# Performance work log

Measured on AMD Instinct MI355X. Metric: run time of the kernel, lower is better.

The kernel has to match this reference:

```python
import jax, jax.numpy as jnp
import numpy as np

B, L, D = 4, 2048, 1024
H, DK, DV, CS = 4, 128, 256, 16  # heads, head_qk_dim, head_v_dim, chunk_size
KD, VD = H * DK, H * DV          # 512, 1024
CONV = 4
EPS = 1e-5


def silu(x):
    return x * jax.nn.sigmoid(x)


def setup_inputs():
    key = jax.random.key(0)
    ks = jax.random.split(key, 9)
    s = 0.02
    return {
        "hidden_states": jax.random.normal(ks[0], (B, L, D), jnp.float32),
        "conv_w": jax.random.normal(ks[1], (D, CONV), jnp.float32) * 0.2,
        "Wq": jax.random.normal(ks[2], (KD, D), jnp.float32) * s,
        "Wk": jax.random.normal(ks[3], (KD, D), jnp.float32) * s,
        "Wv": jax.random.normal(ks[4], (VD, D), jnp.float32) * s,
        "Wb": jax.random.normal(ks[5], (H, D), jnp.float32) * s,
        "Wg": jax.random.normal(ks[6], (VD, D), jnp.float32) * s,
        "Wo": jax.random.normal(ks[7], (D, VD), jnp.float32) * s,
        "norm_w": jnp.ones((DV,), jnp.float32),
    }


def short_conv(x, w):
    # causal depthwise conv1d with SiLU activation: x [B,L,D], w [D,K]
    K = w.shape[1]
    xp = jnp.pad(x, ((0, 0), (K - 1, 0), (0, 0)))
    y = sum(xp[:, j:j + x.shape[1], :] * w[:, j] for j in range(K))
    return silu(y)


def delta_rule_chunk(q, k, v, beta):
    # fused_chunk_delta_rule: q,k [B,H,L,DK], v [B,H,L,DV], beta [B,H,L]
    b, h, l, dk = q.shape
    dv = v.shape[-1]
    nc = l // CS
    k = k * jax.lax.rsqrt(jnp.sum(k * k, -1, keepdims=True) + 1e-12)  # L2-normalize keys
    q = q * (dk ** -0.5)
    qc = q.reshape(b, h, nc, CS, dk)
    kc = k.reshape(b, h, nc, CS, dk)
    vc = v.reshape(b, h, nc, CS, dv)
    bc = beta.reshape(b, h, nc, CS)
    kb = kc * bc[..., None]
    # WY representation: T = (I + strict_tril(diag(beta) K K^T))^{-1}
    A = jnp.einsum('bhncd,bhnmd->bhncm', kb, kc)
    strict = jnp.tril(jnp.ones((CS, CS), q.dtype), -1)
    M = jnp.eye(CS, dtype=q.dtype) + A * strict
    eye = jnp.broadcast_to(jnp.eye(CS, dtype=q.dtype), M.shape)
    T = jax.scipy.linalg.solve_triangular(M, eye, lower=True)
    w = jnp.einsum('bhncm,bhnmd->bhncd', T, kb)
    u = jnp.einsum('bhncm,bhnmd->bhncd', T, vc * bc[..., None])
    causal = jnp.tril(jnp.ones((CS, CS), q.dtype))

    def step(S, inp):
        qi, ki, wi, ui = inp  # [B,H,CS,dk/dv]
        u_adj = ui - jnp.einsum('bhcd,bhdv->bhcv', wi, S)
        attn = jnp.einsum('bhcd,bhmd->bhcm', qi, ki) * causal
        o = jnp.einsum('bhcd,bhdv->bhcv', qi, S) + jnp.einsum('bhcm,bhmv->bhcv', attn, u_adj)
        S = S + jnp.einsum('bhcd,bhcv->bhdv', ki, u_adj)
        return S, o

    xs = tuple(jnp.moveaxis(t, 2, 0) for t in (qc, kc, w, u))
    S0 = jnp.zeros((b, h, dk, dv), q.dtype)
    _, os_ = jax.lax.scan(step, S0, xs)
    return jnp.moveaxis(os_, 0, 2).reshape(b, h, l, dv)


def reference(hidden_states, conv_w, Wq, Wk, Wv, Wb, Wg, Wo, norm_w):
    x = short_conv(hidden_states, conv_w)
    q = (x @ Wq.T).reshape(B, L, H, DK).transpose(0, 2, 1, 3)
    k = (x @ Wk.T).reshape(B, L, H, DK).transpose(0, 2, 1, 3)
    v = (x @ Wv.T).reshape(B, L, H, DV).transpose(0, 2, 1, 3)
    beta = jax.nn.sigmoid(x @ Wb.T).transpose(0, 2, 1)  # [B,H,L]
    o = delta_rule_chunk(q, k, v, beta)                 # [B,H,L,DV]
    o = o.transpose(0, 2, 1, 3)                          # [B,L,H,DV]
    g = (x @ Wg.T).reshape(B, L, H, DV)
    o = o * jax.lax.rsqrt(jnp.mean(o * o, -1, keepdims=True) + EPS) * norm_w * silu(g)
    return o.reshape(B, L, VD) @ Wo.T
```

## Files before the change

kernel.cpp:

```cpp
#include <hip/hip_runtime.h>
#include <cstdint>
#include <cstddef>

typedef _Float16 f16;
typedef _Float16 f16x4 __attribute__((ext_vector_type(4)));
typedef _Float16 f16x8 __attribute__((ext_vector_type(8)));
typedef float floatx4 __attribute__((ext_vector_type(4)));

#define MFMA32(a,b,c) __builtin_amdgcn_mfma_f32_16x16x32_f16((a),(b),(c),0,0,0)

#define ROWS 8192
#define NCHUNK 128
static constexpr float QSCALE = 0.08838834764831845f;

static __device__ __forceinline__ float sigmoidf_(float x) { return 1.0f / (1.0f + expf(-x)); }

static __device__ __forceinline__ uint32_t pack2(f16 a, f16 b) {
  union { f16 h[2]; uint32_t u; } v; v.h[0] = a; v.h[1] = b; return v.u;
}

#define GLOAD_LDS(gptr, lptr)                                                  \
  __builtin_amdgcn_global_load_lds(                                            \
      (const __attribute__((address_space(1))) void*)(gptr),                   \
      (__attribute__((address_space(3))) void*)(lptr), 16, 0, 0)

#define WAITV(N) do { asm volatile("s_waitcnt vmcnt(" #N ")" ::: "memory");    \
                      __builtin_amdgcn_sched_barrier(0); } while (0)

#define SBAR() __builtin_amdgcn_sched_barrier(0)

__global__ __launch_bounds__(256) void wconv_kernel(
    const float* __restrict__ Wq, const float* __restrict__ Wk,
    const float* __restrict__ Wv, const float* __restrict__ Wg,
    const float* __restrict__ Wo,
    f16* __restrict__ WcatHi, f16* __restrict__ WcatLoKV, f16* __restrict__ WoHi) {
  int tid = blockIdx.x * 256 + threadIdx.x;
  int e8 = tid * 8;
  if (e8 < 3145728) {
    int row = e8 >> 10, col = e8 & 1023;
    const float* src;
    if (row < 512)       src = Wk + (size_t)row * 1024 + col;
    else if (row < 1536) src = Wv + (size_t)(row - 512) * 1024 + col;
    else if (row < 2048) src = Wq + (size_t)(row - 1536) * 1024 + col;
    else                 src = Wg + (size_t)(row - 2048) * 1024 + col;
    f16 thi[8] __attribute__((aligned(16)));
    f16 tlo[8] __attribute__((aligned(16)));
#pragma unroll
    for (int j = 0; j < 8; j++) {
      float x = src[j];
      f16 h = (f16)x;
      thi[j] = h;
      tlo[j] = (f16)(x - (float)h);
    }
    *(uint4*)&WcatHi[e8] = *(const uint4*)thi;
    if (row < 1536) *(uint4*)&WcatLoKV[e8] = *(const uint4*)tlo;
  } else {
    int idx = e8 - 3145728;
    f16 t[8] __attribute__((aligned(16)));
#pragma unroll
    for (int j = 0; j < 8; j++) t[j] = (f16)Wo[idx + j];
    *(uint4*)&WoHi[idx] = *(const uint4*)t;
  }
}

__global__ __launch_bounds__(256) void conv_kernel(
    const float* __restrict__ hs, const float* __restrict__ cw,
    f16* __restrict__ xhi, f16* __restrict__ xlo) {
  int row = blockIdx.x;
  int b = row >> 11, l = row & 2047;
  int d = threadIdx.x * 4;
  floatx4 w0 = *(const floatx4*)&cw[(d + 0) * 4];
  floatx4 w1 = *(const floatx4*)&cw[(d + 1) * 4];
  floatx4 w2 = *(const floatx4*)&cw[(d + 2) * 4];
  floatx4 w3 = *(const floatx4*)&cw[(d + 3) * 4];
  floatx4 acc = {0.f, 0.f, 0.f, 0.f};
#pragma unroll
  for (int j = 0; j < 4; j++) {
    int ls = l - 3 + j;
    if (ls < 0) continue;
    floatx4 hv = *(const floatx4*)&hs[(size_t)(b * 2048 + ls) * 1024 + d];
    acc[0] += hv[0] * w0[j];
    acc[1] += hv[1] * w1[j];
    acc[2] += hv[2] * w2[j];
    acc[3] += hv[3] * w3[j];
  }
  f16 ohi[4] __attribute__((aligned(8)));
  f16 olo[4] __attribute__((aligned(8)));
#pragma unroll
  for (int q = 0; q < 4; q++) {
    float y = acc[q] * sigmoidf_(acc[q]);
    f16 h = (f16)y;
    ohi[q] = h;
    olo[q] = (f16)(y - (float)h);
  }
  *(uint2*)&xhi[(size_t)row * 1024 + d] = *(const uint2*)ohi;
  *(uint2*)&xlo[(size_t)row * 1024 + d] = *(const uint2*)olo;
}

__global__ __launch_bounds__(256) void beta_kernel(
    const f16* __restrict__ xhi, const f16* __restrict__ xlo,
    const float* __restrict__ Wb, float* __restrict__ betaf) {
  int row = blockIdx.x;
  int t = threadIdx.x;
  __shared__ floatx4 red[256];
  int c = t * 4;
  float xv[4];
#pragma unroll
  for (int j = 0; j < 4; j++)
    xv[j] = (float)xhi[(size_t)row * 1024 + c + j] + (float)xlo[(size_t)row * 1024 + c + j];
  floatx4 p = {0.f, 0.f, 0.f, 0.f};
#pragma unroll
  for (int hh = 0; hh < 4; hh++) {
    const float* wr = Wb + hh * 1024 + c;
    p[hh] = xv[0] * wr[0] + xv[1] * wr[1] + xv[2] * wr[2] + xv[3] * wr[3];
  }
  red[t] = p;
  __syncthreads();
  for (int s = 128; s > 0; s >>= 1) {
    if (t < s) red[t] += red[t + s];
    __syncthreads();
  }
  if (t < 4) betaf[(size_t)row * 4 + t] = sigmoidf_(red[0][t]);
}

__global__ __launch_bounds__(256) void gemm_hilo_kv(
    const f16* __restrict__ Ahi, const f16* __restrict__ Alo,
    const f16* __restrict__ Bhi, const f16* __restrict__ Blo,
    f16* __restrict__ ChHi, f16* __restrict__ ChLo, int K) {
  __shared__ __attribute__((aligned(16))) f16 AsH[4096];
  __shared__ __attribute__((aligned(16))) f16 AsL[4096];
  __shared__ __attribute__((aligned(16))) f16 BsH[4096];
  __shared__ __attribute__((aligned(16))) f16 BsL[4096];
  const int t = threadIdx.x;
  const int lane = t & 63, wave = t >> 6;
  const int lc = lane & 15, quad = lane >> 4;
  const int wm = (wave >> 1) * 64, wn = (wave & 1) * 64;
  const int m0 = blockIdx.y * 128, n0 = blockIdx.x * 128;
  const int scol = ((lane & 3) ^ ((lane >> 3) & 3)) * 8;
  int srow[2];
#pragma unroll
  for (int pp = 0; pp < 2; pp++) srow[pp] = (wave * 2 + pp) * 16 + (lane >> 2);
  const int swz = (quad ^ ((lc >> 1) & 3)) * 8;
  floatx4 acc[4][4] = {};
  for (int kt = 0; kt < K; kt += 32) {
    __syncthreads();
#pragma unroll
    for (int pp = 0; pp < 2; pp++) {
      int ldso = (wave * 2 + pp) * 512;
      GLOAD_LDS(&Ahi[(size_t)(m0 + srow[pp]) * K + kt + scol], AsH + ldso);
      GLOAD_LDS(&Alo[(size_t)(m0 + srow[pp]) * K + kt + scol], AsL + ldso);
      GLOAD_LDS(&Bhi[(size_t)(n0 + srow[pp]) * K + kt + scol], BsH + ldso);
      GLOAD_LDS(&Blo[(size_t)(n0 + srow[pp]) * K + kt + scol], BsL + ldso);
    }
    __syncthreads();
    f16x8 ah[4], al[4], bh2[4], bl[4];
#pragma unroll
    for (int i = 0; i < 4; i++) {
      ah[i] = *(const f16x8*)&AsH[(wm + i * 16 + lc) * 32 + swz];
      al[i] = *(const f16x8*)&AsL[(wm + i * 16 + lc) * 32 + swz];
    }
#pragma unroll
    for (int j = 0; j < 4; j++) {
      bh2[j] = *(const f16x8*)&BsH[(wn + j * 16 + lc) * 32 + swz];
      bl[j]  = *(const f16x8*)&BsL[(wn + j * 16 + lc) * 32 + swz];
    }
#pragma unroll
    for (int i = 0; i < 4; i++)
#pragma unroll
      for (int j = 0; j < 4; j++) {
        acc[i][j] = MFMA32(ah[i], bh2[j], acc[i][j]);
        acc[i][j] = MFMA32(al[i], bh2[j], acc[i][j]);
        acc[i][j] = MFMA32(ah[i], bl[j], acc[i][j]);
      }
  }
#pragma unroll
  for (int i = 0; i < 4; i++)
#pragma unroll
    for (int j = 0; j < 4; j++)
#pragma unroll
      for (int rr = 0; rr < 4; rr++) {
        int row = m0 + wm + i * 16 + quad * 4 + rr;
        int col = n0 + wn + j * 16 + lc;
        float x = acc[i][j][rr];
        f16 h = (f16)x;
        ChHi[(size_t)row * 3072 + col] = h;
        ChLo[(size_t)row * 1536 + col] = (f16)(x - (float)h);
      }
}

template <int OUTF16>
__global__ __launch_bounds__(256) void gemm_plain(
    const f16* __restrict__ A, const f16* __restrict__ Bw,
    f16* __restrict__ Ch, float* __restrict__ Cf, int K, int ldc) {
  __shared__ __attribute__((aligned(16))) f16 As[4096];
  __shared__ __attribute__((aligned(16))) f16 Bs[4096];
  const int t = threadIdx.x;
  const int lane = t & 63, wave = t >> 6;
  const int lc = lane & 15, quad = lane >> 4;
  const int wm = (wave >> 1) * 64, wn = (wave & 1) * 64;
  const int m0 = blockIdx.y * 128, n0 = blockIdx.x * 128;
  const int scol = ((lane & 3) ^ ((lane >> 3) & 3)) * 8;
  int srow[2];
#pragma unroll
  for (int pp = 0; pp < 2; pp++) srow[pp] = (wave * 2 + pp) * 16 + (lane >> 2);
  const int swz = (quad ^ ((lc >> 1) & 3)) * 8;
  floatx4 acc[4][4] = {};
  for (int kt = 0; kt < K; kt += 32) {
    __syncthreads();
#pragma unroll
    for (int pp = 0; pp < 2; pp++) {
      int ldso = (wave * 2 + pp) * 512;
      GLOAD_LDS(&A[(size_t)(m0 + srow[pp]) * K + kt + scol],  As + ldso);
      GLOAD_LDS(&Bw[(size_t)(n0 + srow[pp]) * K + kt + scol], Bs + ldso);
    }
    __syncthreads();
    f16x8 af[4], bf[4];
#pragma unroll
    for (int i = 0; i < 4; i++) af[i] = *(const f16x8*)&As[(wm + i * 16 + lc) * 32 + swz];
#pragma unroll
    for (int j = 0; j < 4; j++) bf[j] = *(const f16x8*)&Bs[(wn + j * 16 + lc) * 32 + swz];
#pragma unroll
    for (int i = 0; i < 4; i++)
#pragma unroll
      for (int j = 0; j < 4; j++) acc[i][j] = MFMA32(af[i], bf[j], acc[i][j]);
  }
#pragma unroll
  for (int i = 0; i < 4; i++)
#pragma unroll
    for (int j = 0; j < 4; j++)
#pragma unroll
      for (int rr = 0; rr < 4; rr++) {
        int row = m0 + wm + i * 16 + quad * 4 + rr;
        int col = n0 + wn + j * 16 + lc;
        if (OUTF16) Ch[(size_t)row * ldc + col] = (f16)acc[i][j][rr];
        else        Cf[(size_t)row * ldc + col] = acc[i][j][rr];
      }
}

__global__ __launch_bounds__(256) void prepass_kernel(
    const f16* __restrict__ qkvgHi, const f16* __restrict__ kvLo,
    const float* __restrict__ betaf,
    f16* __restrict__ wHi, f16* __restrict__ wLo,
    f16* __restrict__ kTHi, f16* __restrict__ kTLo,
    f16* __restrict__ uHi, f16* __restrict__ uLo,
    float* __restrict__ attno) {
  int bid = blockIdx.x;
  int bh = bid >> 7, n = bid & 127;
  int b = bh >> 2, h = bh & 3;
  int t = threadIdx.x;

  __shared__ __attribute__((aligned(16))) float kc[16][132];
  __shared__ __attribute__((aligned(16))) float qc[16][132];
  __shared__ __attribute__((aligned(16))) float vb[16][260];
  __shared__ float Mm[16][16];
  __shared__ float Tt[16][16];
  __shared__ float Tb[16][16];
  __shared__ float part[16][16];
  __shared__ float betas[16];
  __shared__ float nrm[16];

  const size_t rowbase = (size_t)(b * 2048 + n * 16);
  {
    int i = t >> 4, o8 = (t & 15) * 8;
    size_t oh = (rowbase + i) * 3072;
    size_t ol = (rowbase + i) * 1536;
#pragma unroll
    for (int j = 0; j < 8; j++)
      kc[i][o8 + j] = (float)qkvgHi[oh + h * 128 + o8 + j] +
                      (float)kvLo[ol + h * 128 + o8 + j];
#pragma unroll
    for (int j = 0; j < 8; j++)
      qc[i][o8 + j] = (float)qkvgHi[oh + 1536 + h * 128 + o8 + j];
  }
  if (t < 16) betas[t] = betaf[(rowbase + t) * 4 + h];
  __syncthreads();
  {
    int i = t >> 4, sg = t & 15;
    float s = 0.f;
#pragma unroll
    for (int j = 0; j < 8; j++) { float v = kc[i][sg * 8 + j]; s += v * v; }
    part[i][sg] = s;
  }
  __syncthreads();
  if (t < 16) {
    float s = 0.f;
#pragma unroll
    for (int j = 0; j < 16; j++) s += part[t][j];
    nrm[t] = rsqrtf(s + 1e-12f);
  }
  __syncthreads();
  {
    int i = t >> 4, o8 = (t & 15) * 8;
    float sc = nrm[i];
#pragma unroll
    for (int j = 0; j < 8; j++) kc[i][o8 + j] *= sc;
  }
  __syncthreads();
  {
    int d = t & 127, ih = t >> 7;
    f16 thi[8] __attribute__((aligned(16)));
    f16 tlo[8] __attribute__((aligned(16)));
#pragma unroll
    for (int j = 0; j < 8; j++) {
      float x = kc[ih * 8 + j][d];
      f16 hh = (f16)x;
      thi[j] = hh;
      tlo[j] = (f16)(x - (float)hh);
    }
    size_t base = ((size_t)bh * 128 + n) * 2048 + d * 16 + ih * 8;
    *(uint4*)&kTHi[base] = *(const uint4*)thi;
    *(uint4*)&kTLo[base] = *(const uint4*)tlo;
  }
  {
    int i = t >> 4, j = t & 15;
    float s = 0.f;
    for (int x = 0; x < 128; x += 4)
      s += kc[i][x] * kc[j][x] + kc[i][x + 1] * kc[j][x + 1] +
           kc[i][x + 2] * kc[j][x + 2] + kc[i][x + 3] * kc[j][x + 3];
    Mm[i][j] = (i == j ? 1.f : 0.f) + ((j < i) ? betas[i] * s : 0.f);
  }
  __syncthreads();
  if (t < 16) {
    int j = t;
    float Tc[16];
#pragma unroll
    for (int i = 0; i < 16; i++) Tc[i] = 0.f;
    Tc[j] = 1.f;
    for (int i = j + 1; i < 16; i++) {
      float s = 0.f;
      for (int k2 = j; k2 < i; k2++) s += Mm[i][k2] * Tc[k2];
      Tc[i] = -s;
    }
    for (int i = 0; i < 16; i++) Tt[i][j] = Tc[i];
  }
  __syncthreads();
  { int i = t >> 4, m = t & 15; Tb[i][m] = Tt[i][m] * betas[m]; }
  {
    int m = t >> 4, c16 = (t & 15) * 16;
    size_t oh = (rowbase + m) * 3072 + 512 + h * 256 + c16;
    size_t ol = (rowbase + m) * 1536 + 512 + h * 256 + c16;
    float bm = betas[m];
#pragma unroll
    for (int j = 0; j < 16; j++)
      vb[m][c16 + j] = bm * ((float)qkvgHi[oh + j] + (float)kvLo[ol + j]);
  }
  __syncthreads();
  {
    int i = t >> 4, dg = t & 15;
    f16 thi[8] __attribute__((aligned(16)));
    f16 tlo[8] __attribute__((aligned(16)));
#pragma unroll
    for (int dd = 0; dd < 8; dd++) {
      int d = dg * 8 + dd;
      float s = 0.f;
#pragma unroll
      for (int m = 0; m < 16; m++) s += Tb[i][m] * kc[m][d];
      s = -s;
      f16 hh = (f16)s;
      thi[dd] = hh;
      tlo[dd] = (f16)(s - (float)hh);
    }
    size_t base = ((size_t)bh * 128 + n) * 2048 + i * 128 + dg * 8;
    *(uint4*)&wHi[base] = *(const uint4*)thi;
    *(uint4*)&wLo[base] = *(const uint4*)tlo;
  }
  {
    int v = t;
    f16 thi[16] __attribute__((aligned(16)));
    f16 tlo[16] __attribute__((aligned(16)));
#pragma unroll
    for (int i = 0; i < 16; i++) {
      float s2 = 0.f;
#pragma unroll
      for (int m = 0; m < 16; m++) s2 += Tt[i][m] * vb[m][v];
      f16 hh = (f16)s2;
      thi[i] = hh;
      tlo[i] = (f16)(s2 - (float)hh);
    }
    size_t base = ((((size_t)(v >> 4) * 16 + bh) * 128 + n) * 16 + (v & 15)) * 16;
    ((uint4*)&uHi[base])[0] = ((const uint4*)thi)[0];
    ((uint4*)&uHi[base])[1] = ((const uint4*)thi)[1];
    ((uint4*)&uLo[base])[0] = ((const uint4*)tlo)[0];
    ((uint4*)&uLo[base])[1] = ((const uint4*)tlo)[1];
  }
  {
    int i = t >> 4, j = t & 15;
    float s = 0.f;
    for (int x = 0; x < 128; x++) s += qc[i][x] * kc[j][x];
    attno[((size_t)bh * 128 + n) * 256 + i * 16 + j] = (j <= i) ? QSCALE * s : 0.f;
  }
}

#define STG_W   0
#define STG_WL  2048
#define STG_Q   4096
#define STG_KH  6144
#define STG_KL  8192
#define STG_SZ  10240

__global__ __launch_bounds__(64, 1) void scan_kernel(
    const f16* __restrict__ qkvgHi,
    const f16* __restrict__ wHi, const f16* __restrict__ wLo,
    const f16* __restrict__ kTHi, const f16* __restrict__ kTLo,
    const float* __restrict__ attn,
    const f16* __restrict__ uHi, const f16* __restrict__ uLo,
    float* __restrict__ o1, float* __restrict__ o2) {
  const int bid = blockIdx.x;
  const int slc = bid >> 4, bh = bid & 15;
  const int b = bh >> 2, h = bh & 3;
  const int v0 = slc * 16;
  const int lane = threadIdx.x;
  const int lc = lane & 15, quad = lane >> 4;
  const int qh = quad & 1;

  __shared__ __attribute__((aligned(16))) f16 stg[2][STG_SZ];
  __shared__ __attribute__((aligned(16))) f16 S_hi[16][136];
  __shared__ __attribute__((aligned(16))) f16 S_lo[16][136];

  floatx4 accS[8] = {};

  const size_t cb = (size_t)bh * 128;
  const f16* qb = qkvgHi + (size_t)b * 2048 * 3072 + 1536 + h * 128;
  const f16* ubH = uHi + ((size_t)(slc * 16 + bh)) * 128 * 256 + lc * 16 + quad * 4;
  const f16* ubL = uLo + ((size_t)(slc * 16 + bh)) * 128 * 256 + lc * 16 + quad * 4;
  const float* ab = attn + cb * 256 + lc * 16 + qh * 8;
  float* ob = (bh < 12) ? (o1 + (size_t)bh * 2048 * 256)
                        : (o2 + (size_t)(bh - 12) * 2048 * 256);

  int woff[4], koff[4], qoff[4];
#pragma unroll
  for (int p = 0; p < 4; p++) {
    int cid = p * 64 + lane;
    int row = cid >> 4, dgs = (cid & 15) ^ (row & 7);
    int d = cid >> 1,  ih = (cid & 1) ^ ((cid >> 3) & 1);
    woff[p] = row * 128 + dgs * 8;
    koff[p] = d * 16 + ih * 8;
    qoff[p] = row * 3072 + dgs * 8;
  }

  uint4 pa0[2], pa1[2];
  uint2 puh[2], pul[2];

  auto ISSUE_REG = [&](int slot, int nn) {
    pa0[slot] = *(const uint4*)(ab + (size_t)nn * 256);
    pa1[slot] = *(const uint4*)(ab + (size_t)nn * 256 + 4);
    puh[slot] = *(const uint2*)(ubH + (size_t)nn * 256);
    pul[slot] = *(const uint2*)(ubL + (size_t)nn * 256);
  };
  auto ISSUE_WQ = [&](int buf, int nn) {
    const f16* wsrc  = wHi + (cb + (size_t)nn) * 2048;
    const f16* wlsrc = wLo + (cb + (size_t)nn) * 2048;
    const f16* qsrc  = qb + (size_t)nn * 16 * 3072;
    f16* sbp = &stg[buf][0];
#pragma unroll
    for (int p = 0; p < 4; p++) {
      GLOAD_LDS(wsrc + woff[p],  sbp + STG_W  + p * 512);
      GLOAD_LDS(wlsrc + woff[p], sbp + STG_WL + p * 512);
      GLOAD_LDS(qsrc + qoff[p],  sbp + STG_Q  + p * 512);
    }
  };
  auto ISSUE_K = [&](int buf, int nn) {
    const f16* khsrc = kTHi + (cb + (size_t)nn) * 2048;
    const f16* klsrc = kTLo + (cb + (size_t)nn) * 2048;
    f16* sbp = &stg[buf][0];
#pragma unroll
    for (int p = 0; p < 4; p++) {
      GLOAD_LDS(khsrc + koff[p], sbp + STG_KH + p * 512);
      GLOAD_LDS(klsrc + koff[p], sbp + STG_KL + p * 512);
    }
  };

  ISSUE_REG(0, 0); ISSUE_WQ(0, 0); ISSUE_K(0, 0);
  ISSUE_REG(1, 1); ISSUE_WQ(1, 1); ISSUE_K(1, 1);

  for (int n = 0; n < NCHUNK; n += 2) {
#pragma unroll
    for (int hf = 0; hf < 2; hf++) {
      const int nn = n + hf;
      f16* sb = &stg[hf][0];

#pragma unroll
      for (int dt = 0; dt < 8; dt++) {
        f16x4 h4, l4;
#pragma unroll
        for (int r = 0; r < 4; r++) {
          float x = accS[dt][r];
          f16 hh = (f16)x;
          h4[r] = hh;
          l4[r] = (f16)(x - (float)hh);
        }
        *(f16x4*)&S_hi[lc][dt * 16 + quad * 4] = h4;
        *(f16x4*)&S_lo[lc][dt * 16 + quad * 4] = l4;
      }

      if (nn == 0)       WAITV(24);
      else if (nn < 127) WAITV(28);
      else               WAITV(4);

      floatx4 acc_u;
      {
        union { uint2 u2; f16 hh[4]; } Uh, Ul;
        Uh.u2 = puh[hf]; Ul.u2 = pul[hf];
#pragma unroll
        for (int r = 0; r < 4; r++) acc_u[r] = (float)Uh.hh[r] + (float)Ul.hh[r];
      }
      f16x8 aah, aal;
      {
        union { uint4 u4[2]; float f[8]; } PA;
        PA.u4[0] = pa0[hf]; PA.u4[1] = pa1[hf];
#pragma unroll
        for (int j = 0; j < 8; j++) {
          float a = PA.f[j];
          f16 ahh = (f16)a;
          aah[j] = ahh;
          aal[j] = (f16)(a - (float)ahh);
        }
      }
      if (nn + 2 < NCHUNK) ISSUE_REG(hf, nn + 2);

      f16x8 shf[4], slf[4], wah[4], wal[4], qah[4];
#pragma unroll
      for (int ks = 0; ks < 4; ks++) {
        shf[ks] = *(const f16x8*)&S_hi[lc][ks * 32 + quad * 8];
        slf[ks] = *(const f16x8*)&S_lo[lc][ks * 32 + quad * 8];
        int gi = lc * 128 + (((ks * 4 + quad) ^ (lc & 7)) * 8);
        wah[ks] = *(const f16x8*)(sb + STG_W  + gi);
        wal[ks] = *(const f16x8*)(sb + STG_WL + gi);
        qah[ks] = *(const f16x8*)(sb + STG_Q  + gi);
      }
      SBAR();
      if (nn + 2 < NCHUNK) ISSUE_WQ(hf, nn + 2);

      floatx4 a1 = {0.f, 0.f, 0.f, 0.f}, a2 = {0.f, 0.f, 0.f, 0.f};
#pragma unroll
      for (int ks = 0; ks < 4; ks++) {
        acc_u = MFMA32(wah[ks], shf[ks], acc_u);
        a1    = MFMA32(wah[ks], slf[ks], a1);
        a2    = MFMA32(wal[ks], shf[ks], a2);
      }
      acc_u = acc_u + a1 + a2;
      floatx4 acc_o = {0.f, 0.f, 0.f, 0.f};
#pragma unroll
      for (int ks = 0; ks < 4; ks++) acc_o = MFMA32(qah[ks], shf[ks], acc_o);
#pragma unroll
      for (int ks = 0; ks < 4; ks++) acc_o = MFMA32(qah[ks], slf[ks], acc_o);

      f16x8 ubf;
      {
        f16 h0 = (f16)acc_u[0], h1 = (f16)acc_u[1];
        f16 h2 = (f16)acc_u[2], h3 = (f16)acc_u[3];
        uint32_t uh01 = pack2(h0, h1), uh23 = pack2(h2, h3);
        uint32_t ul01 = pack2((f16)(acc_u[0] - (float)h0), (f16)(acc_u[1] - (float)h1));
        uint32_t ul23 = pack2((f16)(acc_u[2] - (float)h2), (f16)(acc_u[3] - (float)h3));
        int srcA = (2 * qh) * 16 + lc;
        int srcB = srcA + 16;
        uint32_t Ah0 = __shfl((int)uh01, srcA, 64), Ah1 = __shfl((int)uh23, srcA, 64);
        uint32_t Bh0 = __shfl((int)uh01, srcB, 64), Bh1 = __shfl((int)uh23, srcB, 64);
        uint32_t Al0 = __shfl((int)ul01, srcA, 64), Al1 = __shfl((int)ul23, srcA, 64);
        uint32_t Bl0 = __shfl((int)ul01, srcB, 64), Bl1 = __shfl((int)ul23, srcB, 64);
        union { uint32_t u[4]; f16x8 v; } U;
        bool hi = (quad < 2);
        U.u[0] = hi ? Ah0 : Al0;
        U.u[1] = hi ? Ah1 : Al1;
        U.u[2] = hi ? Bh0 : Bl0;
        U.u[3] = hi ? Bh1 : Bl1;
        ubf = U.v;
      }
#pragma unroll
      for (int r = 0; r < 4; r++) acc_o[r] *= QSCALE;
      acc_o = MFMA32(aah, ubf, acc_o);
      acc_o = MFMA32(aal, ubf, acc_o);
#pragma unroll
      for (int r = 0; r < 4; r++)
        ob[(size_t)(nn * 16 + quad * 4 + r) * 256 + v0 + lc] = acc_o[r];

      const int kswz = (qh ^ ((lc >> 2) & 1)) * 8 + lc * 16;
#pragma unroll
      for (int dt = 0; dt < 8; dt++) {
        f16x8 kah = *(const f16x8*)(sb + STG_KH + dt * 256 + kswz);
        f16x8 kal = *(const f16x8*)(sb + STG_KL + dt * 256 + kswz);
        accS[dt] = MFMA32(kah, ubf, accS[dt]);
        accS[dt] = MFMA32(kal, ubf, accS[dt]);
      }
      SBAR();
      if (nn + 2 < NCHUNK) ISSUE_K(hf, nn + 2);
    }
  }
}

__global__ __launch_bounds__(256) void gate_kernel(
    const float* __restrict__ o1, const float* __restrict__ o2,
    const f16* __restrict__ qkvgHi, const float* __restrict__ norm_w,
    f16* __restrict__ onh) {
  int h = threadIdx.x >> 6, lane = threadIdx.x & 63;
  int r = blockIdx.x;
  int b = r >> 11, l = r & 2047;
  int bh = b * 4 + h;
  const float* orow = ((bh < 12) ? (o1 + (size_t)bh * 524288)
                                 : (o2 + (size_t)(bh - 12) * 524288)) + (size_t)l * 256;
  int v = lane * 4;
  floatx4 ov = *(const floatx4*)&orow[v];
  float ss = ov[0] * ov[0] + ov[1] * ov[1] + ov[2] * ov[2] + ov[3] * ov[3];
  for (int m = 32; m > 0; m >>= 1) ss += __shfl_xor(ss, m);
  float rms = rsqrtf(ss * (1.0f / 256.0f) + 1e-5f);
  size_t goff = (size_t)r * 3072 + 2048 + h * 256 + v;
  floatx4 nw = *(const floatx4*)&norm_w[v];
  f16 outv[4] __attribute__((aligned(8)));
#pragma unroll
  for (int q2 = 0; q2 < 4; q2++) {
    float g = (float)qkvgHi[goff + q2];
    outv[q2] = (f16)(ov[q2] * rms * nw[q2] * (g * sigmoidf_(g)));
  }
  *(uint2*)&onh[(size_t)r * 1024 + h * 256 + v] = *(const uint2*)outv;
}

extern "C" void kernel_launch(void* const* d_in, const int* in_sizes, int n_in,
                              void* d_out, int out_size, void* d_ws, size_t ws_size,
                              hipStream_t stream) {
  (void)in_sizes; (void)n_in; (void)out_size; (void)ws_size;
  const float* hs     = (const float*)d_in[0];
  const float* conv_w = (const float*)d_in[1];
  const float* Wq     = (const float*)d_in[2];
  const float* Wk     = (const float*)d_in[3];
  const float* Wv     = (const float*)d_in[4];
  const float* Wb     = (const float*)d_in[5];
  const float* Wg     = (const float*)d_in[6];
  const float* Wo     = (const float*)d_in[7];
  const float* norm_w = (const float*)d_in[8];
  float* out = (float*)d_out;

  char* ws = (char*)d_ws;
  f16*   x_hi    = (f16*)(ws + 0);
  f16*   x_lo    = (f16*)(ws + 16777216);
  f16*   uHi     = (f16*)(ws + 0);
  f16*   uLo     = (f16*)(ws + 16777216);
  f16*   WcatHi  = (f16*)(ws + 33554432);
  float* o2f     = (float*)(ws + 33554432);
  f16*   WcatLo  = (f16*)(ws + 39845888);
  f16*   WoHi    = (f16*)(ws + 42991616);
  float* betaf   = (float*)(ws + 45088768);
  f16*   qkvgHi  = (f16*)(ws + 45219840);
  f16*   kvLo    = (f16*)(ws + 95551488);
  float* o1f     = (float*)(ws + 95551488);
  f16*   wHi     = (f16*)(ws + 120717312);
  f16*   on_h    = (f16*)(ws + 120717312);
  f16*   wLo     = (f16*)(ws + 129105920);
  f16*   kTHi    = (f16*)(ws + 137494528);
  f16*   kTLo    = (f16*)(ws + 145883136);
  float* attnf   = (float*)(ws + 154271744);

  wconv_kernel<<<2048, 256, 0, stream>>>(Wq, Wk, Wv, Wg, Wo, WcatHi, WcatLo, WoHi);
  conv_kernel<<<ROWS, 256, 0, stream>>>(hs, conv_w, x_hi, x_lo);
  beta_kernel<<<ROWS, 256, 0, stream>>>(x_hi, x_lo, Wb, betaf);
  gemm_hilo_kv<<<dim3(12, 64), 256, 0, stream>>>(
      x_hi, x_lo, WcatHi, WcatLo, qkvgHi, kvLo, 1024);
  gemm_plain<1><<<dim3(12, 64), 256, 0, stream>>>(
      x_hi, WcatHi + (size_t)1536 * 1024, qkvgHi + 1536, nullptr, 1024, 3072);
  prepass_kernel<<<16 * NCHUNK, 256, 0, stream>>>(
      qkvgHi, kvLo, betaf, wHi, wLo, kTHi, kTLo, uHi, uLo, attnf);
  scan_kernel<<<256, 64, 0, stream>>>(
      qkvgHi, wHi, wLo, kTHi, kTLo, attnf, uHi, uLo, o1f, o2f);
  gate_kernel<<<ROWS, 256, 0, stream>>>(o1f, o2f, qkvgHi, norm_w, on_h);
  gemm_plain<0><<<dim3(8, 64), 256, 0, stream>>>(
      on_h, WoHi, nullptr, out, 1024, 1024);
}
```

Measured before the change: 567.7 us.

## Process chunk pairs per scan step using precomputed cross-chunk correction matrices

```diff
diff --git a/kernel.cpp b/kernel.cpp
--- a/kernel.cpp
+++ b/kernel.cpp
@@ -11,6 +11,7 @@
 
 #define ROWS 8192
 #define NCHUNK 128
+#define NSUPER 64
 static constexpr float QSCALE = 0.08838834764831845f;
 
 static __device__ __forceinline__ float sigmoidf_(float x) { return 1.0f / (1.0f + expf(-x)); }
@@ -391,12 +392,55 @@
   }
 }
 
+__global__ __launch_bounds__(256) void cabd_kernel(
+    f16* qkvg,
+    const f16* __restrict__ wHi, const f16* __restrict__ wLo,
+    const f16* __restrict__ kTHi, const f16* __restrict__ kTLo) {
+  int bid = blockIdx.x;
+  int bh = bid >> 6, sc = bid & 63;
+  int b = bh >> 2, h = bh & 3;
+  int t = threadIdx.x;
+  int cA = 2 * sc, cB = 2 * sc + 1;
+  const size_t cb = (size_t)bh * 128;
+
+  __shared__ float wf[16][128];
+  __shared__ float qf[16][128];
+  __shared__ float kf[128][17];
+
+  {
+    int i = t >> 4, d0 = (t & 15) * 8;
+    size_t wbase = (cb + cB) * 2048 + i * 128 + d0;
+    size_t qbase = ((size_t)b * 2048 + cB * 16 + i) * 3072 + 1536 + h * 128 + d0;
+#pragma unroll
+    for (int j = 0; j < 8; j++) {
+      wf[i][d0 + j] = (float)wHi[wbase + j] + (float)wLo[wbase + j];
+      qf[i][d0 + j] = (float)qkvg[qbase + j];
+    }
+    int d = t >> 1, tk0 = (t & 1) * 8;
+    size_t kb = (cb + cA) * 2048 + d * 16 + tk0;
+#pragma unroll
+    for (int j = 0; j < 8; j++)
+      kf[d][tk0 + j] = (float)kTHi[kb + j] + (float)kTLo[kb + j];
+  }
+  __syncthreads();
+  int i = t >> 4, j = t & 15;
+  float sc1 = 0.f, sd1 = 0.f;
+  for (int d = 0; d < 128; d++) {
+    float kv = kf[d][j];
+    sc1 += wf[i][d] * kv;
+    sd1 += qf[i][d] * kv;
+  }
+  f16 ch = (f16)sc1, dh = (f16)sd1;
+  size_t o = (size_t)(bh * 64 + sc) * 3072 + 512 + i * 16 + j;
+  qkvg[o]       = ch;  qkvg[o + 256] = (f16)(sc1 - (float)ch);
+  qkvg[o + 512] = dh;  qkvg[o + 768] = (f16)(sd1 - (float)dh);
+}
+
 #define STG_W   0
 #define STG_WL  2048
-#define STG_Q   4096
-#define STG_KH  6144
-#define STG_KL  8192
-#define STG_SZ  10240
+#define STG_KH  4096
+#define STG_KL  6144
+#define STG_CH  8192
 
 __global__ __launch_bounds__(64, 1) void scan_kernel(
     const f16* __restrict__ qkvgHi,
@@ -413,7 +457,7 @@
   const int lc = lane & 15, quad = lane >> 4;
   const int qh = quad & 1;
 
-  __shared__ __attribute__((aligned(16))) f16 stg[2][STG_SZ];
+  __shared__ __attribute__((aligned(16))) f16 stg[2][STG_CH];
   __shared__ __attribute__((aligned(16))) f16 S_hi[16][136];
   __shared__ __attribute__((aligned(16))) f16 S_lo[16][136];
 
@@ -421,13 +465,14 @@
 
   const size_t cb = (size_t)bh * 128;
   const f16* qb = qkvgHi + (size_t)b * 2048 * 3072 + 1536 + h * 128;
-  const f16* ubH = uHi + ((size_t)(slc * 16 + bh)) * 128 * 256 + lc * 16 + quad * 4;
-  const f16* ubL = uLo + ((size_t)(slc * 16 + bh)) * 128 * 256 + lc * 16 + quad * 4;
+  const f16* ubH = uHi + ((size_t)(slc * 16 + bh)) * 32768 + lc * 16 + quad * 4;
+  const f16* ubL = uLo + ((size_t)(slc * 16 + bh)) * 32768 + lc * 16 + quad * 4;
   const float* ab = attn + cb * 256 + lc * 16 + qh * 8;
+  const f16* cd = qkvgHi + (size_t)(bh * 64) * 3072 + 512 + lc * 16 + qh * 8;
   float* ob = (bh < 12) ? (o1 + (size_t)bh * 2048 * 256)
                         : (o2 + (size_t)(bh - 12) * 2048 * 256);
 
-  int woff[4], koff[4], qoff[4];
+  int woff[4], koff[4];
 #pragma unroll
   for (int p = 0; p < 4; p++) {
     int cid = p * 64 + lane;
@@ -435,49 +480,88 @@
     int d = cid >> 1,  ih = (cid & 1) ^ ((cid >> 3) & 1);
     woff[p] = row * 128 + dgs * 8;
     koff[p] = d * 16 + ih * 8;
-    qoff[p] = row * 3072 + dgs * 8;
-  }
-
-  uint4 pa0[2], pa1[2];
-  uint2 puh[2], pul[2];
-
-  auto ISSUE_REG = [&](int slot, int nn) {
-    pa0[slot] = *(const uint4*)(ab + (size_t)nn * 256);
-    pa1[slot] = *(const uint4*)(ab + (size_t)nn * 256 + 4);
-    puh[slot] = *(const uint2*)(ubH + (size_t)nn * 256);
-    pul[slot] = *(const uint2*)(ubL + (size_t)nn * 256);
+  }
+
+  uint2 puhA[2], pulA[2], puhB[2], pulB[2];
+
+  auto ISSUE_U = [&](int slot, int sc) {
+    puhA[slot] = *(const uint2*)(ubH + (size_t)(2 * sc) * 256);
+    pulA[slot] = *(const uint2*)(ubL + (size_t)(2 * sc) * 256);
+    puhB[slot] = *(const uint2*)(ubH + (size_t)(2 * sc + 1) * 256);
+    pulB[slot] = *(const uint2*)(ubL + (size_t)(2 * sc + 1) * 256);
   };
-  auto ISSUE_WQ = [&](int buf, int nn) {
-    const f16* wsrc  = wHi + (cb + (size_t)nn) * 2048;
-    const f16* wlsrc = wLo + (cb + (size_t)nn) * 2048;
-    const f16* qsrc  = qb + (size_t)nn * 16 * 3072;
-    f16* sbp = &stg[buf][0];
-#pragma unroll
-    for (int p = 0; p < 4; p++) {
-      GLOAD_LDS(wsrc + woff[p],  sbp + STG_W  + p * 512);
-      GLOAD_LDS(wlsrc + woff[p], sbp + STG_WL + p * 512);
-      GLOAD_LDS(qsrc + qoff[p],  sbp + STG_Q  + p * 512);
+  auto ISSUE_W = [&](int sc) {
+#pragma unroll
+    for (int ci = 0; ci < 2; ci++) {
+      const f16* ws = wHi + (cb + (size_t)(2 * sc + ci)) * 2048;
+      const f16* wl = wLo + (cb + (size_t)(2 * sc + ci)) * 2048;
+      f16* sbp = &stg[ci][0];
+#pragma unroll
+      for (int p = 0; p < 4; p++) {
+        GLOAD_LDS(ws + woff[p], sbp + STG_W  + p * 512);
+        GLOAD_LDS(wl + woff[p], sbp + STG_WL + p * 512);
+      }
     }
   };
-  auto ISSUE_K = [&](int buf, int nn) {
-    const f16* khsrc = kTHi + (cb + (size_t)nn) * 2048;
-    const f16* klsrc = kTLo + (cb + (size_t)nn) * 2048;
-    f16* sbp = &stg[buf][0];
-#pragma unroll
-    for (int p = 0; p < 4; p++) {
-      GLOAD_LDS(khsrc + koff[p], sbp + STG_KH + p * 512);
-      GLOAD_LDS(klsrc + koff[p], sbp + STG_KL + p * 512);
+  auto ISSUE_K = [&](int sc) {
+#pragma unroll
+    for (int ci = 0; ci < 2; ci++) {
+      const f16* kh = kTHi + (cb + (size_t)(2 * sc + ci)) * 2048;
+      const f16* kl = kTLo + (cb + (size_t)(2 * sc + ci)) * 2048;
+      f16* sbp = &stg[ci][0];
+#pragma unroll
+      for (int p = 0; p < 4; p++) {
+        GLOAD_LDS(kh + koff[p], sbp + STG_KH + p * 512);
+        GLOAD_LDS(kl + koff[p], sbp + STG_KL + p * 512);
+      }
     }
   };
 
-  ISSUE_REG(0, 0); ISSUE_WQ(0, 0); ISSUE_K(0, 0);
-  ISSUE_REG(1, 1); ISSUE_WQ(1, 1); ISSUE_K(1, 1);
-
-  for (int n = 0; n < NCHUNK; n += 2) {
-#pragma unroll
-    for (int hf = 0; hf < 2; hf++) {
-      const int nn = n + hf;
-      f16* sb = &stg[hf][0];
+  auto SHFL_EXCH = [&](floatx4 acc_u) -> f16x8 {
+    f16 h0 = (f16)acc_u[0], h1 = (f16)acc_u[1];
+    f16 h2 = (f16)acc_u[2], h3 = (f16)acc_u[3];
+    uint32_t uh01 = pack2(h0, h1), uh23 = pack2(h2, h3);
+    uint32_t ul01 = pack2((f16)(acc_u[0] - (float)h0), (f16)(acc_u[1] - (float)h1));
+    uint32_t ul23 = pack2((f16)(acc_u[2] - (float)h2), (f16)(acc_u[3] - (float)h3));
+    int srcA = (2 * qh) * 16 + lc;
+    int srcB = srcA + 16;
+    uint32_t Ah0 = __shfl((int)uh01, srcA, 64), Ah1 = __shfl((int)uh23, srcA, 64);
+    uint32_t Bh0 = __shfl((int)uh01, srcB, 64), Bh1 = __shfl((int)uh23, srcB, 64);
+    uint32_t Al0 = __shfl((int)ul01, srcA, 64), Al1 = __shfl((int)ul23, srcA, 64);
+    uint32_t Bl0 = __shfl((int)ul01, srcB, 64), Bl1 = __shfl((int)ul23, srcB, 64);
+    union { uint32_t u[4]; f16x8 v; } U;
+    bool hi = (quad < 2);
+    U.u[0] = hi ? Ah0 : Al0;
+    U.u[1] = hi ? Ah1 : Al1;
+    U.u[2] = hi ? Bh0 : Bl0;
+    U.u[3] = hi ? Bh1 : Bl1;
+    return U.v;
+  };
+
+  auto ATTN_SPLIT = [&](uint4 p0, uint4 p1, f16x8& hh, f16x8& ll) {
+    union { uint4 u4[2]; float f[8]; } PA;
+    PA.u4[0] = p0; PA.u4[1] = p1;
+#pragma unroll
+    for (int j = 0; j < 8; j++) {
+      float a = PA.f[j];
+      f16 ah = (f16)a;
+      hh[j] = ah;
+      ll[j] = (f16)(a - (float)ah);
+    }
+  };
+
+  const int kswz = (qh ^ ((lc >> 2) & 1)) * 8 + lc * 16;
+
+  ISSUE_U(0, 0); SBAR();
+  ISSUE_W(0);    SBAR();
+  ISSUE_K(0);    SBAR();
+
+  for (int s2 = 0; s2 < NSUPER; s2 += 2) {
+#pragma unroll
+    for (int half = 0; half < 2; half++) {
+      const int sc = s2 + half;
+      const int slot = half;
+      const int cA = 2 * sc;
 
 #pragma unroll
       for (int dt = 0; dt < 8; dt++) {
@@ -493,97 +577,142 @@
         *(f16x4*)&S_lo[lc][dt * 16 + quad * 4] = l4;
       }
 
-      if (nn == 0)       WAITV(24);
-      else if (nn < 127) WAITV(28);
-      else               WAITV(4);
-
-      floatx4 acc_u;
+      WAITV(16);
+
+      uint4 paA0 = *(const uint4*)(ab + (size_t)cA * 256);
+      uint4 paA1 = *(const uint4*)(ab + (size_t)cA * 256 + 4);
+      uint4 paB0 = *(const uint4*)(ab + (size_t)(cA + 1) * 256);
+      uint4 paB1 = *(const uint4*)(ab + (size_t)(cA + 1) * 256 + 4);
+      const f16* cdp = cd + (size_t)sc * 3072;
+      f16x8 cabh = *(const f16x8*)(cdp);
+      f16x8 cabl = *(const f16x8*)(cdp + 256);
+      f16x8 dbah = *(const f16x8*)(cdp + 512);
+      f16x8 dbal = *(const f16x8*)(cdp + 768);
+      f16x8 qfA[4], qfB[4];
+#pragma unroll
+      for (int ks = 0; ks < 4; ks++) {
+        qfA[ks] = *(const f16x8*)(qb + (size_t)(cA * 16 + lc) * 3072 + ks * 32 + quad * 8);
+        qfB[ks] = *(const f16x8*)(qb + (size_t)((cA + 1) * 16 + lc) * 3072 + ks * 32 + quad * 8);
+      }
+      SBAR();
+
+      floatx4 acc_uA, acc_uB;
       {
         union { uint2 u2; f16 hh[4]; } Uh, Ul;
-        Uh.u2 = puh[hf]; Ul.u2 = pul[hf];
-#pragma unroll
-        for (int r = 0; r < 4; r++) acc_u[r] = (float)Uh.hh[r] + (float)Ul.hh[r];
-      }
-      f16x8 aah, aal;
-      {
-        union { uint4 u4[2]; float f[8]; } PA;
-        PA.u4[0] = pa0[hf]; PA.u4[1] = pa1[hf];
-#pragma unroll
-        for (int j = 0; j < 8; j++) {
-          float a = PA.f[j];
-          f16 ahh = (f16)a;
-          aah[j] = ahh;
-          aal[j] = (f16)(a - (float)ahh);
-        }
-      }
-      if (nn + 2 < NCHUNK) ISSUE_REG(hf, nn + 2);
-
-      f16x8 shf[4], slf[4], wah[4], wal[4], qah[4];
+        Uh.u2 = puhA[slot]; Ul.u2 = pulA[slot];
+#pragma unroll
+        for (int r = 0; r < 4; r++) acc_uA[r] = (float)Uh.hh[r] + (float)Ul.hh[r];
+        Uh.u2 = puhB[slot]; Ul.u2 = pulB[slot];
+#pragma unroll
+        for (int r = 0; r < 4; r++) acc_uB[r] = (float)Uh.hh[r] + (float)Ul.hh[r];
+      }
+      if (sc + 1 < NSUPER) ISSUE_U(slot ^ 1, sc + 1);
+      SBAR();
+
+      f16x8 shf[4], slf[4], wah[4], wal[4];
+      f16* sbA = &stg[0][0];
+      f16* sbB = &stg[1][0];
 #pragma unroll
       for (int ks = 0; ks < 4; ks++) {
         shf[ks] = *(const f16x8*)&S_hi[lc][ks * 32 + quad * 8];
         slf[ks] = *(const f16x8*)&S_lo[lc][ks * 32 + quad * 8];
         int gi = lc * 128 + (((ks * 4 + quad) ^ (lc & 7)) * 8);
-        wah[ks] = *(const f16x8*)(sb + STG_W  + gi);
-        wal[ks] = *(const f16x8*)(sb + STG_WL + gi);
-        qah[ks] = *(const f16x8*)(sb + STG_Q  + gi);
-      }
+        wah[ks] = *(const f16x8*)(sbA + STG_W  + gi);
+        wal[ks] = *(const f16x8*)(sbA + STG_WL + gi);
+      }
+      floatx4 a1 = {0.f,0.f,0.f,0.f}, a2 = {0.f,0.f,0.f,0.f};
+#pragma unroll
+      for (int ks = 0; ks < 4; ks++) {
+        acc_uA = MFMA32(wah[ks], shf[ks], acc_uA);
+        a1     = MFMA32(wah[ks], slf[ks], a1);
+        a2     = MFMA32(wal[ks], shf[ks], a2);
+      }
+      acc_uA = acc_uA + a1 + a2;
+
+      f16x8 wbh[4], wbl[4];
+#pragma unroll
+      for (int ks = 0; ks < 4; ks++) {
+        int gi = lc * 128 + (((ks * 4 + quad) ^ (lc & 7)) * 8);
+        wbh[ks] = *(const f16x8*)(sbB + STG_W  + gi);
+        wbl[ks] = *(const f16x8*)(sbB + STG_WL + gi);
+      }
+      floatx4 b1 = {0.f,0.f,0.f,0.f}, b2 = {0.f,0.f,0.f,0.f};
+#pragma unroll
+      for (int ks = 0; ks < 4; ks++) {
+        acc_uB = MFMA32(wbh[ks], shf[ks], acc_uB);
+        b1     = MFMA32(wbh[ks], slf[ks], b1);
+        b2     = MFMA32(wbl[ks], shf[ks], b2);
+      }
+      acc_uB = acc_uB + b1 + b2;
       SBAR();
-      if (nn + 2 < NCHUNK) ISSUE_WQ(hf, nn + 2);
-
-      floatx4 a1 = {0.f, 0.f, 0.f, 0.f}, a2 = {0.f, 0.f, 0.f, 0.f};
+      if (sc + 1 < NSUPER) ISSUE_W(sc + 1);
+      SBAR();
+
+      floatx4 acc_oA = {0.f,0.f,0.f,0.f}, acc_oB = {0.f,0.f,0.f,0.f};
 #pragma unroll
       for (int ks = 0; ks < 4; ks++) {
-        acc_u = MFMA32(wah[ks], shf[ks], acc_u);
-        a1    = MFMA32(wah[ks], slf[ks], a1);
-        a2    = MFMA32(wal[ks], shf[ks], a2);
-      }
-      acc_u = acc_u + a1 + a2;
-      floatx4 acc_o = {0.f, 0.f, 0.f, 0.f};
-#pragma unroll
-      for (int ks = 0; ks < 4; ks++) acc_o = MFMA32(qah[ks], shf[ks], acc_o);
-#pragma unroll
-      for (int ks = 0; ks < 4; ks++) acc_o = MFMA32(qah[ks], slf[ks], acc_o);
-
-      f16x8 ubf;
+        acc_oA = MFMA32(qfA[ks], shf[ks], acc_oA);
+        acc_oB = MFMA32(qfB[ks], shf[ks], acc_oB);
+      }
+#pragma unroll
+      for (int ks = 0; ks < 4; ks++) {
+        acc_oA = MFMA32(qfA[ks], slf[ks], acc_oA);
+        acc_oB = MFMA32(qfB[ks], slf[ks], acc_oB);
+      }
+
+      f16x8 ubfA = SHFL_EXCH(acc_uA);
+
+      acc_uB = MFMA32(cabh, ubfA, acc_uB);
+      acc_uB = MFMA32(cabl, ubfA, acc_uB);
+      acc_oB = MFMA32(dbah, ubfA, acc_oB);
+      acc_oB = MFMA32(dbal, ubfA, acc_oB);
+
       {
-        f16 h0 = (f16)acc_u[0], h1 = (f16)acc_u[1];
-        f16 h2 = (f16)acc_u[2], h3 = (f16)acc_u[3];
-        uint32_t uh01 = pack2(h0, h1), uh23 = pack2(h2, h3);
-        uint32_t ul01 = pack2((f16)(acc_u[0] - (float)h0), (f16)(acc_u[1] - (float)h1));
-        uint32_t ul23 = pack2((f16)(acc_u[2] - (float)h2), (f16)(acc_u[3] - (float)h3));
-        int srcA = (2 * qh) * 16 + lc;
-        int srcB = srcA + 16;
-        uint32_t Ah0 = __shfl((int)uh01, srcA, 64), Ah1 = __shfl((int)uh23, srcA, 64);
-        uint32_t Bh0 = __shfl((int)uh01, srcB, 64), Bh1 = __shfl((int)uh23, srcB, 64);
-        uint32_t Al0 = __shfl((int)ul01, srcA, 64), Al1 = __shfl((int)ul23, srcA, 64);
-        uint32_t Bl0 = __shfl((int)ul01, srcB, 64), Bl1 = __shfl((int)ul23, srcB, 64);
-        union { uint32_t u[4]; f16x8 v; } U;
-        bool hi = (quad < 2);
-        U.u[0] = hi ? Ah0 : Al0;
-        U.u[1] = hi ? Ah1 : Al1;
-        U.u[2] = hi ? Bh0 : Bl0;
-        U.u[3] = hi ? Bh1 : Bl1;
-        ubf = U.v;
-      }
-#pragma unroll
-      for (int r = 0; r < 4; r++) acc_o[r] *= QSCALE;
-      acc_o = MFMA32(aah, ubf, acc_o);
-      acc_o = MFMA32(aal, ubf, acc_o);
+        f16x8 aah, aal;
+        ATTN_SPLIT(paA0, paA1, aah, aal);
+#pragma unroll
+        for (int r = 0; r < 4; r++) acc_oA[r] *= QSCALE;
+        acc_oA = MFMA32(aah, ubfA, acc_oA);
+        acc_oA = MFMA32(aal, ubfA, acc_oA);
+      }
 #pragma unroll
       for (int r = 0; r < 4; r++)
-        ob[(size_t)(nn * 16 + quad * 4 + r) * 256 + v0 + lc] = acc_o[r];
-
-      const int kswz = (qh ^ ((lc >> 2) & 1)) * 8 + lc * 16;
+        ob[(size_t)(cA * 16 + quad * 4 + r) * 256 + v0 + lc] = acc_oA[r];
+      SBAR();
+
+      f16x8 ubfB = SHFL_EXCH(acc_uB);
+      {
+        f16x8 bah, bal;
+        ATTN_SPLIT(paB0, paB1, bah, bal);
+#pragma unroll
+        for (int r = 0; r < 4; r++) acc_oB[r] *= QSCALE;
+        acc_oB = MFMA32(bah, ubfB, acc_oB);
+        acc_oB = MFMA32(bal, ubfB, acc_oB);
+      }
+#pragma unroll
+      for (int r = 0; r < 4; r++)
+        ob[(size_t)((cA + 1) * 16 + quad * 4 + r) * 256 + v0 + lc] = acc_oB[r];
+      SBAR();
+
+      if (sc + 1 < NSUPER) { WAITV(44); } else { WAITV(24); }
+
 #pragma unroll
       for (int dt = 0; dt < 8; dt++) {
-        f16x8 kah = *(const f16x8*)(sb + STG_KH + dt * 256 + kswz);
-        f16x8 kal = *(const f16x8*)(sb + STG_KL + dt * 256 + kswz);
-        accS[dt] = MFMA32(kah, ubf, accS[dt]);
-        accS[dt] = MFMA32(kal, ubf, accS[dt]);
+        f16x8 kah = *(const f16x8*)(sbA + STG_KH + dt * 256 + kswz);
+        f16x8 kal = *(const f16x8*)(sbA + STG_KL + dt * 256 + kswz);
+        accS[dt] = MFMA32(kah, ubfA, accS[dt]);
+        accS[dt] = MFMA32(kal, ubfA, accS[dt]);
+      }
+#pragma unroll
+      for (int dt = 0; dt < 8; dt++) {
+        f16x8 kbh = *(const f16x8*)(sbB + STG_KH + dt * 256 + kswz);
+        f16x8 kbl = *(const f16x8*)(sbB + STG_KL + dt * 256 + kswz);
+        accS[dt] = MFMA32(kbh, ubfB, accS[dt]);
+        accS[dt] = MFMA32(kbl, ubfB, accS[dt]);
       }
       SBAR();
-      if (nn + 2 < NCHUNK) ISSUE_K(hf, nn + 2);
+      if (sc + 1 < NSUPER) ISSUE_K(sc + 1);
+      SBAR();
     }
   }
 }
@@ -658,6 +787,8 @@
       x_hi, WcatHi + (size_t)1536 * 1024, qkvgHi + 1536, nullptr, 1024, 3072);
   prepass_kernel<<<16 * NCHUNK, 256, 0, stream>>>(
       qkvgHi, kvLo, betaf, wHi, wLo, kTHi, kTLo, uHi, uLo, attnf);
+  cabd_kernel<<<16 * NSUPER, 256, 0, stream>>>(
+      qkvgHi, wHi, wLo, kTHi, kTLo);
   scan_kernel<<<256, 64, 0, stream>>>(
       qkvgHi, wHi, wLo, kTHi, kTLo, attnf, uHi, uLo, o1f, o2f);
   gate_kernel<<<ROWS, 256, 0, stream>>>(o1f, o2f, qkvgHi, norm_w, on_h);
```

Result: slower. 579.1 us (+2.0%).
